# Performance work log

Measured on AMD Instinct MI355X. Metric: run time of the kernel, lower is better.

The kernel has to match this reference:

```python
import jax, jax.numpy as jnp
import numpy as np

Q_DIM, V_DIM, HID = 768, 512, 512


def setup_inputs() -> dict:
    key = jax.random.key(0)
    kV, kQ, kwq, kbq, kwv, kbv = jax.random.split(key, 6)
    B, Nv, Nq = 64, 1024, 512
    V = jax.random.normal(kV, (B, Nv, V_DIM), dtype=jnp.float32)
    Q = jax.random.normal(kQ, (B, Nq, Q_DIM), dtype=jnp.float32)
    # torch Linear params: weight [out, in], bias [out]
    Wq_w = jax.random.normal(kwq, (HID, Q_DIM), dtype=jnp.float32) / np.sqrt(Q_DIM)
    Wq_b = jax.random.normal(kbq, (HID,), dtype=jnp.float32) * 0.01
    Wv_w = jax.random.normal(kwv, (HID, V_DIM), dtype=jnp.float32) / np.sqrt(V_DIM)
    Wv_b = jax.random.normal(kbv, (HID,), dtype=jnp.float32) * 0.01
    return {"V": V, "Q": Q, "Wq_w": Wq_w, "Wq_b": Wq_b, "Wv_w": Wv_w, "Wv_b": Wv_b}


def reference(V, Q, Wq_w, Wq_b, Wv_w, Wv_b):
    # Q_proj: [B, Nq, HID]; V_proj: [B, Nv, HID]
    Q_proj = jnp.einsum('bqd,hd->bqh', Q, Wq_w) + Wq_b
    V_proj = jnp.einsum('bvd,hd->bvh', V, Wv_w) + Wv_b
    # H: [B, Nq, Nv]
    H = jnp.tanh(jnp.einsum('bqh,bvh->bqv', Q_proj, V_proj))
    A_v = jax.nn.softmax(H, axis=2)              # over Nv
    V_tilde = jnp.einsum('bqv,bvd->bqd', A_v, V)  # [B, Nq, V_DIM]
    A_q = jax.nn.softmax(H, axis=1)              # softmax(H^T, dim=2) == softmax over Nq
    Q_tilde = jnp.einsum('bqv,bqd->bvd', A_q, Q)  # [B, Nv, Q_DIM]
    v_hat = V_tilde.sum(axis=1)                   # [B, V_DIM]
    q_hat = Q_tilde.sum(axis=1)                   # [B, Q_DIM]
    return (v_hat, q_hat)
```

## Files before the change

### kernel.cpp

```cpp
#include <hip/hip_runtime.h>
#include <hip/hip_bf16.h>
#include <math.h>

#define B_SZ 64
#define NQ   512
#define NV   1024
#define QD   768
#define VD   512
#define HIDD 512

typedef __bf16 bf16x8 __attribute__((ext_vector_type(8)));
typedef __bf16 bf16x4 __attribute__((ext_vector_type(4)));
typedef float  floatx4 __attribute__((ext_vector_type(4)));

__device__ __forceinline__ void g2lds16(const __bf16* g, __bf16* l) {
    __builtin_amdgcn_global_load_lds((const __attribute__((address_space(1))) void*)g,
                                     (__attribute__((address_space(3))) void*)l,
                                     16, 0, 0);
}

__device__ __forceinline__ float exptanh(float s) {
    float t = __expf(2.0f * s);
    float r = __builtin_amdgcn_rcpf(t + 1.0f);
    return __expf(1.0f - 2.0f * r);
}

__device__ __forceinline__ void lds_barrier() {
    asm volatile("s_waitcnt lgkmcnt(0)" ::: "memory");
    __builtin_amdgcn_sched_barrier(0);
    __builtin_amdgcn_s_barrier();
}

__global__ __launch_bounds__(256) void cvtpack_k(const float* __restrict__ wq,
                                                 const float* __restrict__ wv,
                                                 __bf16* __restrict__ dq,
                                                 __bf16* __restrict__ dv) {
    const int i = blockIdx.x * 256 + threadIdx.x;
    const int nq8 = (HIDD * QD) / 8;
    const float* W; __bf16* d; int K, o;
    if (i < nq8) { W = wq; d = dq; K = QD; o = i * 8; }
    else         { W = wv; d = dv; K = VD; o = (i - nq8) * 8; }
    const int step = o >> 14;
    const int rem  = o & 16383;
    const int R    = rem >> 5;
    const int qsw  = (rem >> 3) & 3;
    const int q    = qsw ^ ((R >> 1) & 3);
    const float* src = W + (size_t)R * K + step * 32 + q * 8;
    float4 f0 = *(const float4*)src;
    float4 f1 = *(const float4*)(src + 4);
    bf16x8 pk;
    pk[0] = (__bf16)f0.x; pk[1] = (__bf16)f0.y; pk[2] = (__bf16)f0.z; pk[3] = (__bf16)f0.w;
    pk[4] = (__bf16)f1.x; pk[5] = (__bf16)f1.y; pk[6] = (__bf16)f1.z; pk[7] = (__bf16)f1.w;
    *(bf16x8*)(d + o) = pk;
}

__global__ __launch_bounds__(512, 2) void proj_k(
    const float* __restrict__ Qin, const float* __restrict__ Vin,
    const __bf16* __restrict__ Wqpk, const __bf16* __restrict__ Wvpk,
    const float* __restrict__ bq, const float* __restrict__ bv,
    __bf16* __restrict__ Qp, __bf16* __restrict__ Vp)
{
    __shared__ __bf16 As[2][128 * 32];
    __shared__ __bf16 Bs[2][512 * 32];
    const int nqblk = (B_SZ * NQ) / 128;
    const float* A; const __bf16* Wpk; const float* bias; __bf16* Cout; int K, mblk;
    if ((int)blockIdx.x < nqblk) {
        A = Qin; Wpk = Wqpk; bias = bq; Cout = Qp; K = QD; mblk = blockIdx.x;
    } else {
        A = Vin; Wpk = Wvpk; bias = bv; Cout = Vp; K = VD; mblk = blockIdx.x - nqblk;
    }
    const int nsteps = K / 32;

    const int t = threadIdx.x, lane = t & 63, wave = t >> 6;
    const int fr = lane & 15, quad = lane >> 4;
    const int fo = (quad ^ ((fr >> 1) & 3)) * 8;
    const int tile_m = mblk * 128;
    const int wm = (wave >> 2) * 64;
    const int wn = (wave & 3) * 128;

    const int arow = t >> 2, aslot = t & 3;
    const float* ap = A + (size_t)(tile_m + arow) * K + aslot * 8;
    const int awoff = arow * 32 + ((aslot ^ ((arow >> 1) & 3)) * 8);
    const __bf16* wp = Wpk + t * 8;

    floatx4 acc[4][8] = {};
    bf16x8 wr0, wr1, wr2, wr3;
    float4 af0, af1;

    auto loadW = [&](int s) {
        const __bf16* p = wp + (size_t)s * 16384;
        wr0 = *(const bf16x8*)(p);
        wr1 = *(const bf16x8*)(p + 4096);
        wr2 = *(const bf16x8*)(p + 8192);
        wr3 = *(const bf16x8*)(p + 12288);
    };
    auto loadA = [&](int s) {
        af0 = *(const float4*)(ap + s * 32);
        af1 = *(const float4*)(ap + s * 32 + 4);
    };
    auto stage = [&](int p) {
        *(bf16x8*)&Bs[p][t * 8]         = wr0;
        *(bf16x8*)&Bs[p][4096 + t * 8]  = wr1;
        *(bf16x8*)&Bs[p][8192 + t * 8]  = wr2;
        *(bf16x8*)&Bs[p][12288 + t * 8] = wr3;
        bf16x8 pk;
        pk[0] = (__bf16)af0.x; pk[1] = (__bf16)af0.y; pk[2] = (__bf16)af0.z; pk[3] = (__bf16)af0.w;
        pk[4] = (__bf16)af1.x; pk[5] = (__bf16)af1.y; pk[6] = (__bf16)af1.z; pk[7] = (__bf16)af1.w;
        *(bf16x8*)&As[p][awoff] = pk;
    };
    auto compute = [&](int p) {
        bf16x8 af[4];
        #pragma unroll
        for (int i = 0; i < 4; i++)
            af[i] = *(const bf16x8*)&As[p][(wm + 16 * i + fr) * 32 + fo];
        #pragma unroll
        for (int j = 0; j < 8; j++) {
            bf16x8 bg = *(const bf16x8*)&Bs[p][(wn + 16 * j + fr) * 32 + fo];
            #pragma unroll
            for (int i = 0; i < 4; i++)
                acc[i][j] = __builtin_amdgcn_mfma_f32_16x16x32_bf16(af[i], bg, acc[i][j], 0, 0, 0);
        }
    };

    loadW(0); loadA(0);
    stage(0);
    loadW(1); loadA(1);
    lds_barrier();

    int cur = 0;
    for (int s = 0; s < nsteps - 2; ++s) {
        stage(cur ^ 1);
        loadW(s + 2); loadA(s + 2);
        compute(cur);
        lds_barrier();
        cur ^= 1;
    }
    stage(cur ^ 1);
    compute(cur);
    lds_barrier();
    cur ^= 1;
    compute(cur);

    #pragma unroll
    for (int j = 0; j < 8; j++) {
        const int col = wn + 16 * j + fr;
        const float bvv = bias[col];
        #pragma unroll
        for (int i = 0; i < 4; i++)
            #pragma unroll
            for (int r = 0; r < 4; r++) {
                const int row = tile_m + wm + 16 * i + quad * 4 + r;
                Cout[(size_t)row * HIDD + col] = (__bf16)(acc[i][j][r] + bvv);
            }
    }
}

__global__ __launch_bounds__(256, 2) void gemm_h(
    const __bf16* __restrict__ Qp, const __bf16* __restrict__ Vp,
    __bf16* __restrict__ Eg, float* __restrict__ R, float* __restrict__ Csum)
{
    __shared__ __bf16 As[2][128 * 32];
    __shared__ __bf16 Bs[2][256 * 32];
    const int b      = blockIdx.z;
    const int tile_q = blockIdx.y * 128;
    const int tile_v = blockIdx.x * 256;
    const int t = threadIdx.x, lane = t & 63, wave = t >> 6;
    const int fr = lane & 15, quad = lane >> 4;
    const int fo   = (quad ^ ((fr >> 1) & 3)) * 8;
    const int gksw = ((lane & 3) ^ ((lane >> 3) & 3)) * 8;
    const int wm = (wave >> 1) * 64, wn = (wave & 1) * 128;

    const __bf16* Aq = Qp + ((size_t)b * NQ + tile_q + wave * 16 + (lane >> 2)) * HIDD + gksw;
    const __bf16* Bv = Vp + ((size_t)b * NV + tile_v + wave * 16 + (lane >> 2)) * HIDD + gksw;

    auto stage = [&](int p, int k0) {
        #pragma unroll
        for (int c = 0; c < 2; c++)
            g2lds16(Aq + (size_t)(c * 64) * HIDD + k0, &As[p][(c * 64 + wave * 16) * 32]);
        #pragma unroll
        for (int c = 0; c < 4; c++)
            g2lds16(Bv + (size_t)(c * 64) * HIDD + k0, &Bs[p][(c * 64 + wave * 16) * 32]);
    };

    floatx4 acc[4][8] = {};
    auto compute = [&](int p) {
        bf16x8 af[4];
        #pragma unroll
        for (int i = 0; i < 4; i++)
            af[i] = *(const bf16x8*)&As[p][(wm + 16 * i + fr) * 32 + fo];
        #pragma unroll
        for (int j = 0; j < 8; j++) {
            bf16x8 bg = *(const bf16x8*)&Bs[p][(wn + 16 * j + fr) * 32 + fo];
            #pragma unroll
            for (int i = 0; i < 4; i++)
                acc[i][j] = __builtin_amdgcn_mfma_f32_16x16x32_bf16(af[i], bg, acc[i][j], 0, 0, 0);
        }
    };

    stage(0, 0);
    __syncthreads();
    int cur = 0;
    for (int k0 = 32; k0 < HIDD; k0 += 32) {
        stage(cur ^ 1, k0);
        compute(cur);
        __syncthreads();
        cur ^= 1;
    }
    compute(cur);

    #pragma unroll
    for (int i = 0; i < 4; i++)
        #pragma unroll
        for (int j = 0; j < 8; j++)
            #pragma unroll
            for (int r = 0; r < 4; r++)
                acc[i][j][r] = exptanh(acc[i][j][r]);

    #pragma unroll
    for (int i = 0; i < 4; i++)
        #pragma unroll
        for (int r = 0; r < 4; r++) {
            const size_t rowbase =
                ((size_t)b * NQ + tile_q + wm + 16 * i + quad * 4 + r) * NV + tile_v;
            #pragma unroll
            for (int j = 0; j < 8; j++)
                Eg[rowbase + wn + 16 * j + fr] = (__bf16)acc[i][j][r];
        }

    #pragma unroll
    for (int i = 0; i < 4; i++)
        #pragma unroll
        for (int r = 0; r < 4; r++) {
            float s = 0.f;
            #pragma unroll
            for (int j = 0; j < 8; j++) s += acc[i][j][r];
            s += __shfl_xor(s, 1); s += __shfl_xor(s, 2);
            s += __shfl_xor(s, 4); s += __shfl_xor(s, 8);
            if (fr == 0)
                atomicAdd(&R[b * NQ + tile_q + wm + 16 * i + quad * 4 + r], s);
        }
    #pragma unroll
    for (int j = 0; j < 8; j++) {
        float s = 0.f;
        #pragma unroll
        for (int i = 0; i < 4; i++)
            #pragma unroll
            for (int r = 0; r < 4; r++) s += acc[i][j][r];
        s += __shfl_xor(s, 16); s += __shfl_xor(s, 32);
        if (quad == 0)
            atomicAdd(&Csum[b * NV + tile_v + wn + 16 * j + fr], s);
    }
}

__global__ __launch_bounds__(512) void marg_k(
    const __bf16* __restrict__ E, const float* __restrict__ R,
    const float* __restrict__ C, float* __restrict__ sv,
    float* __restrict__ sq)
{
    __shared__ float sred[8][1024];
    const int b  = blockIdx.y;
    const int q0 = blockIdx.x * 64;
    const int t = threadIdx.x, lane = t & 63, wave = t >> 6;
    const float* Cb = C + b * NV;
    float ci[2][8];
    float svp[2][8] = {};
    #pragma unroll
    for (int c = 0; c < 2; c++) {
        float4 c0 = *(const float4*)&Cb[c * 512 + lane * 8];
        float4 c1 = *(const float4*)&Cb[c * 512 + lane * 8 + 4];
        ci[c][0] = 1.0f / c0.x; ci[c][1] = 1.0f / c0.y;
        ci[c][2] = 1.0f / c0.z; ci[c][3] = 1.0f / c0.w;
        ci[c][4] = 1.0f / c1.x; ci[c][5] = 1.0f / c1.y;
        ci[c][6] = 1.0f / c1.z; ci[c][7] = 1.0f / c1.w;
    }
    const float* Rb = R + b * NQ + q0 + wave * 8;
    const __bf16* Ebase = E + ((size_t)b * NQ + q0 + wave * 8) * NV;
    #pragma unroll
    for (int rr = 0; rr < 8; rr++) {
        const __bf16* Erow = Ebase + (size_t)rr * NV;
        const float ri = 1.0f / Rb[rr];
        float p = 0.f;
        #pragma unroll
        for (int c = 0; c < 2; c++) {
            bf16x8 ev = *(const bf16x8*)&Erow[c * 512 + lane * 8];
            #pragma unroll
            for (int k = 0; k < 8; k++) {
                float e = (float)ev[k];
                svp[c][k] += e * ri;
                p += e * ci[c][k];
            }
        }
        p += __shfl_xor(p, 1);  p += __shfl_xor(p, 2);  p += __shfl_xor(p, 4);
        p += __shfl_xor(p, 8);  p += __shfl_xor(p, 16); p += __shfl_xor(p, 32);
        if (lane == 0) sq[b * NQ + q0 + wave * 8 + rr] = p;
    }
    #pragma unroll
    for (int c = 0; c < 2; c++) {
        float4 w0 = { svp[c][0], svp[c][1], svp[c][2], svp[c][3] };
        float4 w1 = { svp[c][4], svp[c][5], svp[c][6], svp[c][7] };
        *(float4*)&sred[wave][c * 512 + lane * 8]     = w0;
        *(float4*)&sred[wave][c * 512 + lane * 8 + 4] = w1;
    }
    __syncthreads();
    const int v = t * 2;
    float s0 = 0.f, s1 = 0.f;
    #pragma unroll
    for (int w = 0; w < 8; w++) { s0 += sred[w][v]; s1 += sred[w][v + 1]; }
    atomicAdd(&sv[b * NV + v],     s0);
    atomicAdd(&sv[b * NV + v + 1], s1);
}

__global__ __launch_bounds__(512) void vhat_k(const float* __restrict__ sv,
                                              const float* __restrict__ V,
                                              float* __restrict__ vh_part) {
    __shared__ float svl[256];
    __shared__ float4 red[4][128];
    const int b  = blockIdx.y;
    const int v0 = blockIdx.x * 256;
    const int t  = threadIdx.x;
    if (t < 256) svl[t] = sv[b * NV + v0 + t];
    __syncthreads();
    const int g = t >> 7, gi = t & 127;
    const float* Vb = V + ((size_t)b * NV + v0 + g) * VD + gi * 4;
    float4 a = {0.f, 0.f, 0.f, 0.f};
    #pragma unroll 8
    for (int i = 0; i < 64; i++) {
        const float s = svl[g + 4 * i];
        const float4 x = *(const float4*)(Vb + (size_t)(4 * i) * VD);
        a.x += s * x.x; a.y += s * x.y; a.z += s * x.z; a.w += s * x.w;
    }
    red[g][gi] = a;
    __syncthreads();
    if (t < 128) {
        float4 r0 = red[0][t], r1 = red[1][t], r2 = red[2][t], r3 = red[3][t];
        float4 o;
        o.x = r0.x + r1.x + r2.x + r3.x;
        o.y = r0.y + r1.y + r2.y + r3.y;
        o.z = r0.z + r1.z + r2.z + r3.z;
        o.w = r0.w + r1.w + r2.w + r3.w;
        *(float4*)&vh_part[((size_t)blockIdx.x * B_SZ + b) * VD + t * 4] = o;
    }
}

__global__ __launch_bounds__(384) void qhat_k(const float* __restrict__ sq,
                                              const float* __restrict__ Q,
                                              float* __restrict__ qh_part) {
    __shared__ float sql[128];
    __shared__ float4 red[2][192];
    const int b  = blockIdx.y;
    const int q0 = blockIdx.x * 128;
    const int t  = threadIdx.x;
    if (t < 128) sql[t] = sq[b * NQ + q0 + t];
    __syncthreads();
    const int g = (t >= 192) ? 1 : 0, gi = t - g * 192;
    const float* Qb = Q + ((size_t)b * NQ + q0 + g) * QD + gi * 4;
    float4 a = {0.f, 0.f, 0.f, 0.f};
    #pragma unroll 8
    for (int i = 0; i < 64; i++) {
        const float s = sql[g + 2 * i];
        const float4 x = *(const float4*)(Qb + (size_t)(2 * i) * QD);
        a.x += s * x.x; a.y += s * x.y; a.z += s * x.z; a.w += s * x.w;
    }
    red[g][gi] = a;
    __syncthreads();
    if (t < 192) {
        float4 r0 = red[0][t], r1 = red[1][t];
        float4 o;
        o.x = r0.x + r1.x; o.y = r0.y + r1.y;
        o.z = r0.z + r1.z; o.w = r0.w + r1.w;
        *(float4*)&qh_part[((size_t)blockIdx.x * B_SZ + b) * QD + t * 4] = o;
    }
}

__global__ __launch_bounds__(256) void fin_k(const float* __restrict__ vh_part,
                                             const float* __restrict__ qh_part,
                                             float* __restrict__ out) {
    const int i = blockIdx.x * 256 + threadIdx.x;
    const int nv = B_SZ * VD;
    const int nq = B_SZ * QD;
    if (i < nv) {
        float s = 0.f;
        #pragma unroll
        for (int p = 0; p < 4; p++) s += vh_part[(size_t)p * nv + i];
        out[i] = s;
    } else if (i < nv + nq) {
        const int j = i - nv;
        float s = 0.f;
        #pragma unroll
        for (int p = 0; p < 4; p++) s += qh_part[(size_t)p * nq + j];
        out[i] = s;
    }
}

extern "C" void kernel_launch(void* const* d_in, const int* in_sizes, int n_in,
                              void* d_out, int out_size, void* d_ws, size_t ws_size,
                              hipStream_t stream) {
    const float* V    = (const float*)d_in[0];
    const float* Q    = (const float*)d_in[1];
    const float* Wq_w = (const float*)d_in[2];
    const float* Wq_b = (const float*)d_in[3];
    const float* Wv_w = (const float*)d_in[4];
    const float* Wv_b = (const float*)d_in[5];
    float* out = (float*)d_out;

    const size_t nQp = (size_t)B_SZ * NQ * HIDD;
    const size_t nVp = (size_t)B_SZ * NV * HIDD;
    const size_t nE  = (size_t)B_SZ * NQ * NV;
    const size_t nWq = (size_t)HIDD * QD;
    const size_t nWv = (size_t)HIDD * VD;
    __bf16* Qp = (__bf16*)d_ws;
    __bf16* Vp = Qp + nQp;
    __bf16* E  = Vp + nVp;
    float* R   = (float*)(E + nE);
    float* C   = R + (size_t)B_SZ * NQ;
    float* sv  = C + (size_t)B_SZ * NV;
    float* sq  = sv + (size_t)B_SZ * NV;
    __bf16* Wq = (__bf16*)(sq + (size_t)B_SZ * NQ);
    __bf16* Wv = Wq + nWq;
    float* vh_part = (float*)Wq;
    float* qh_part = vh_part + (size_t)4 * B_SZ * VD;
    size_t need = (nQp + nVp + nE + nWq + nWv) * 2 +
                  ((size_t)B_SZ * (NQ + NV) * 2) * 4;
    if (ws_size < need) return;

    hipMemsetAsync(R, 0, ((size_t)B_SZ * (NQ + 2 * NV)) * sizeof(float), stream);

    cvtpack_k<<<(int)((nWq + nWv) / 8 / 256), 256, 0, stream>>>(Wq_w, Wv_w, Wq, Wv);

    proj_k<<<(B_SZ * NQ) / 128 + (B_SZ * NV) / 128, 512, 0, stream>>>(
        Q, V, Wq, Wv, Wq_b, Wv_b, Qp, Vp);

    gemm_h<<<dim3(NV / 256, NQ / 128, B_SZ), 256, 0, stream>>>(Qp, Vp, E, R, C);

    marg_k<<<dim3(NQ / 64, B_SZ), 512, 0, stream>>>(E, R, C, sv, sq);

    vhat_k<<<dim3(NV / 256, B_SZ), 512, 0, stream>>>(sv, V, vh_part);
    qhat_k<<<dim3(NQ / 128, B_SZ), 384, 0, stream>>>(sq, Q, qh_part);

    fin_k<<<(B_SZ * (VD + QD) + 255) / 256, 256, 0, stream>>>(vh_part, qh_part, out);
}
```

Before: 446.3 us.

## Halve per-wave tiles in projection and H GEMMs to raise occupancy

The projection kernel's M tile drops from 128 to 64 rows and the occupancy hint rises to 4 blocks per CU. The H GEMM moves from 256 to 512 threads with 32-row wave tiles. It also replaces direct global-to-LDS loads with register-staged loads that are software-pipelined two steps ahead behind explicit LDS barriers. The aim is to hide memory latency with more resident waves and fewer accumulator registers, at the cost of lower per-wave MFMA reuse and more blocks reloading the weights.

```diff
diff --git a/kernel.cpp b/kernel.cpp
--- a/kernel.cpp
+++ b/kernel.cpp
@@ -12,12 +12,6 @@
 typedef __bf16 bf16x8 __attribute__((ext_vector_type(8)));
 typedef __bf16 bf16x4 __attribute__((ext_vector_type(4)));
 typedef float  floatx4 __attribute__((ext_vector_type(4)));
-
-__device__ __forceinline__ void g2lds16(const __bf16* g, __bf16* l) {
-    __builtin_amdgcn_global_load_lds((const __attribute__((address_space(1))) void*)g,
-                                     (__attribute__((address_space(3))) void*)l,
-                                     16, 0, 0);
-}
 
 __device__ __forceinline__ float exptanh(float s) {
     float t = __expf(2.0f * s);
@@ -54,15 +48,15 @@
     *(bf16x8*)(d + o) = pk;
 }
 
-__global__ __launch_bounds__(512, 2) void proj_k(
+__global__ __launch_bounds__(512, 4) void proj_k(
     const float* __restrict__ Qin, const float* __restrict__ Vin,
     const __bf16* __restrict__ Wqpk, const __bf16* __restrict__ Wvpk,
     const float* __restrict__ bq, const float* __restrict__ bv,
     __bf16* __restrict__ Qp, __bf16* __restrict__ Vp)
 {
-    __shared__ __bf16 As[2][128 * 32];
+    __shared__ __bf16 As[2][64 * 32];
     __shared__ __bf16 Bs[2][512 * 32];
-    const int nqblk = (B_SZ * NQ) / 128;
+    const int nqblk = (B_SZ * NQ) / 64;
     const float* A; const __bf16* Wpk; const float* bias; __bf16* Cout; int K, mblk;
     if ((int)blockIdx.x < nqblk) {
         A = Qin; Wpk = Wqpk; bias = bq; Cout = Qp; K = QD; mblk = blockIdx.x;
@@ -74,18 +68,18 @@
     const int t = threadIdx.x, lane = t & 63, wave = t >> 6;
     const int fr = lane & 15, quad = lane >> 4;
     const int fo = (quad ^ ((fr >> 1) & 3)) * 8;
-    const int tile_m = mblk * 128;
-    const int wm = (wave >> 2) * 64;
+    const int tile_m = mblk * 64;
+    const int wm = (wave >> 2) * 32;
     const int wn = (wave & 3) * 128;
 
-    const int arow = t >> 2, aslot = t & 3;
-    const float* ap = A + (size_t)(tile_m + arow) * K + aslot * 8;
-    const int awoff = arow * 32 + ((aslot ^ ((arow >> 1) & 3)) * 8);
+    const int arow = t >> 3, aq = (t >> 1) & 3, ah = t & 1;
+    const float* ap = A + (size_t)(tile_m + arow) * K + aq * 8 + ah * 4;
+    const int awoff = arow * 32 + ((aq ^ ((arow >> 1) & 3)) * 8) + ah * 4;
     const __bf16* wp = Wpk + t * 8;
 
-    floatx4 acc[4][8] = {};
+    floatx4 acc[2][8] = {};
     bf16x8 wr0, wr1, wr2, wr3;
-    float4 af0, af1;
+    float4 af;
 
     auto loadW = [&](int s) {
         const __bf16* p = wp + (size_t)s * 16384;
@@ -95,30 +89,29 @@
         wr3 = *(const bf16x8*)(p + 12288);
     };
     auto loadA = [&](int s) {
-        af0 = *(const float4*)(ap + s * 32);
-        af1 = *(const float4*)(ap + s * 32 + 4);
+        af = *(const float4*)(ap + s * 32);
     };
     auto stage = [&](int p) {
         *(bf16x8*)&Bs[p][t * 8]         = wr0;
         *(bf16x8*)&Bs[p][4096 + t * 8]  = wr1;
         *(bf16x8*)&Bs[p][8192 + t * 8]  = wr2;
         *(bf16x8*)&Bs[p][12288 + t * 8] = wr3;
-        bf16x8 pk;
-        pk[0] = (__bf16)af0.x; pk[1] = (__bf16)af0.y; pk[2] = (__bf16)af0.z; pk[3] = (__bf16)af0.w;
-        pk[4] = (__bf16)af1.x; pk[5] = (__bf16)af1.y; pk[6] = (__bf16)af1.z; pk[7] = (__bf16)af1.w;
-        *(bf16x8*)&As[p][awoff] = pk;
+        bf16x4 pk;
+        pk[0] = (__bf16)af.x; pk[1] = (__bf16)af.y;
+        pk[2] = (__bf16)af.z; pk[3] = (__bf16)af.w;
+        *(bf16x4*)&As[p][awoff] = pk;
     };
     auto compute = [&](int p) {
-        bf16x8 af[4];
-        #pragma unroll
-        for (int i = 0; i < 4; i++)
-            af[i] = *(const bf16x8*)&As[p][(wm + 16 * i + fr) * 32 + fo];
+        bf16x8 afr[2];
+        #pragma unroll
+        for (int i = 0; i < 2; i++)
+            afr[i] = *(const bf16x8*)&As[p][(wm + 16 * i + fr) * 32 + fo];
         #pragma unroll
         for (int j = 0; j < 8; j++) {
             bf16x8 bg = *(const bf16x8*)&Bs[p][(wn + 16 * j + fr) * 32 + fo];
             #pragma unroll
-            for (int i = 0; i < 4; i++)
-                acc[i][j] = __builtin_amdgcn_mfma_f32_16x16x32_bf16(af[i], bg, acc[i][j], 0, 0, 0);
+            for (int i = 0; i < 2; i++)
+                acc[i][j] = __builtin_amdgcn_mfma_f32_16x16x32_bf16(afr[i], bg, acc[i][j], 0, 0, 0);
         }
     };
 
@@ -146,7 +139,7 @@
         const int col = wn + 16 * j + fr;
         const float bvv = bias[col];
         #pragma unroll
-        for (int i = 0; i < 4; i++)
+        for (int i = 0; i < 2; i++)
             #pragma unroll
             for (int r = 0; r < 4; r++) {
                 const int row = tile_m + wm + 16 * i + quad * 4 + r;
@@ -155,7 +148,7 @@
     }
 }
 
-__global__ __launch_bounds__(256, 2) void gemm_h(
+__global__ __launch_bounds__(512, 4) void gemm_h(
     const __bf16* __restrict__ Qp, const __bf16* __restrict__ Vp,
     __bf16* __restrict__ Eg, float* __restrict__ R, float* __restrict__ Csum)
 {
@@ -166,50 +159,62 @@
     const int tile_v = blockIdx.x * 256;
     const int t = threadIdx.x, lane = t & 63, wave = t >> 6;
     const int fr = lane & 15, quad = lane >> 4;
-    const int fo   = (quad ^ ((fr >> 1) & 3)) * 8;
-    const int gksw = ((lane & 3) ^ ((lane >> 3) & 3)) * 8;
-    const int wm = (wave >> 1) * 64, wn = (wave & 1) * 128;
-
-    const __bf16* Aq = Qp + ((size_t)b * NQ + tile_q + wave * 16 + (lane >> 2)) * HIDD + gksw;
-    const __bf16* Bv = Vp + ((size_t)b * NV + tile_v + wave * 16 + (lane >> 2)) * HIDD + gksw;
-
-    auto stage = [&](int p, int k0) {
-        #pragma unroll
-        for (int c = 0; c < 2; c++)
-            g2lds16(Aq + (size_t)(c * 64) * HIDD + k0, &As[p][(c * 64 + wave * 16) * 32]);
-        #pragma unroll
-        for (int c = 0; c < 4; c++)
-            g2lds16(Bv + (size_t)(c * 64) * HIDD + k0, &Bs[p][(c * 64 + wave * 16) * 32]);
-    };
-
-    floatx4 acc[4][8] = {};
+    const int fo = (quad ^ ((fr >> 1) & 3)) * 8;
+    const int wm = (wave >> 1) * 32, wn = (wave & 1) * 128;
+
+    const int srow = t >> 2;
+    const int scol = ((t & 3) ^ ((srow >> 1) & 3)) * 8;
+    const __bf16* aps = Qp + ((size_t)b * NQ + tile_q + srow) * HIDD + scol;
+    const __bf16* bps = Vp + ((size_t)b * NV + tile_v + srow) * HIDD + scol;
+    const __bf16* bps2 = bps + (size_t)128 * HIDD;
+
+    floatx4 acc[2][8] = {};
+    bf16x8 ar, br0, br1;
+
+    auto loadAB = [&](int s) {
+        ar  = *(const bf16x8*)(aps  + s * 32);
+        br0 = *(const bf16x8*)(bps  + s * 32);
+        br1 = *(const bf16x8*)(bps2 + s * 32);
+    };
+    auto stage = [&](int p) {
+        *(bf16x8*)&As[p][t * 8]        = ar;
+        *(bf16x8*)&Bs[p][t * 8]        = br0;
+        *(bf16x8*)&Bs[p][4096 + t * 8] = br1;
+    };
     auto compute = [&](int p) {
-        bf16x8 af[4];
-        #pragma unroll
-        for (int i = 0; i < 4; i++)
-            af[i] = *(const bf16x8*)&As[p][(wm + 16 * i + fr) * 32 + fo];
+        bf16x8 afr[2];
+        #pragma unroll
+        for (int i = 0; i < 2; i++)
+            afr[i] = *(const bf16x8*)&As[p][(wm + 16 * i + fr) * 32 + fo];
         #pragma unroll
         for (int j = 0; j < 8; j++) {
             bf16x8 bg = *(const bf16x8*)&Bs[p][(wn + 16 * j + fr) * 32 + fo];
             #pragma unroll
-            for (int i = 0; i < 4; i++)
-                acc[i][j] = __builtin_amdgcn_mfma_f32_16x16x32_bf16(af[i], bg, acc[i][j], 0, 0, 0);
+            for (int i = 0; i < 2; i++)
+                acc[i][j] = __builtin_amdgcn_mfma_f32_16x16x32_bf16(afr[i], bg, acc[i][j], 0, 0, 0);
         }
     };
 
-    stage(0, 0);
-    __syncthreads();
+    loadAB(0);
+    stage(0);
+    loadAB(1);
+    lds_barrier();
     int cur = 0;
-    for (int k0 = 32; k0 < HIDD; k0 += 32) {
-        stage(cur ^ 1, k0);
+    for (int s = 0; s < (HIDD / 32) - 2; ++s) {
+        stage(cur ^ 1);
+        loadAB(s + 2);
         compute(cur);
-        __syncthreads();
+        lds_barrier();
         cur ^= 1;
     }
+    stage(cur ^ 1);
     compute(cur);
-
-    #pragma unroll
-    for (int i = 0; i < 4; i++)
+    lds_barrier();
+    cur ^= 1;
+    compute(cur);
+
+    #pragma unroll
+    for (int i = 0; i < 2; i++)
         #pragma unroll
         for (int j = 0; j < 8; j++)
             #pragma unroll
@@ -217,7 +222,7 @@
                 acc[i][j][r] = exptanh(acc[i][j][r]);
 
     #pragma unroll
-    for (int i = 0; i < 4; i++)
+    for (int i = 0; i < 2; i++)
         #pragma unroll
         for (int r = 0; r < 4; r++) {
             const size_t rowbase =
@@ -228,7 +233,7 @@
         }
 
     #pragma unroll
-    for (int i = 0; i < 4; i++)
+    for (int i = 0; i < 2; i++)
         #pragma unroll
         for (int r = 0; r < 4; r++) {
             float s = 0.f;
@@ -243,7 +248,7 @@
     for (int j = 0; j < 8; j++) {
         float s = 0.f;
         #pragma unroll
-        for (int i = 0; i < 4; i++)
+        for (int i = 0; i < 2; i++)
             #pragma unroll
             for (int r = 0; r < 4; r++) s += acc[i][j][r];
         s += __shfl_xor(s, 16); s += __shfl_xor(s, 32);
@@ -427,10 +432,10 @@
 
     cvtpack_k<<<(int)((nWq + nWv) / 8 / 256), 256, 0, stream>>>(Wq_w, Wv_w, Wq, Wv);
 
-    proj_k<<<(B_SZ * NQ) / 128 + (B_SZ * NV) / 128, 512, 0, stream>>>(
+    proj_k<<<(B_SZ * NQ) / 64 + (B_SZ * NV) / 64, 512, 0, stream>>>(
         Q, V, Wq, Wv, Wq_b, Wv_b, Qp, Vp);
 
-    gemm_h<<<dim3(NV / 256, NQ / 128, B_SZ), 256, 0, stream>>>(Qp, Vp, E, R, C);
+    gemm_h<<<dim3(NV / 256, NQ / 128, B_SZ), 512, 0, stream>>>(Qp, Vp, E, R, C);
 
     marg_k<<<dim3(NQ / 64, B_SZ), 512, 0, stream>>>(E, R, C, sv, sq);
 
```

Measured after the change: 439.7 us. About the same (-1.5%).
